# Optimization experiments

Measured on AMD Instinct MI355X. Metric: run time of the kernel, lower is better.

## Reference

```python
import jax, jax.numpy as jnp
import numpy as np
from jax import lax

RADIUS = 4
HIDDEN = 64
CORR_CH = (2 * RADIUS + 1) ** 2  # 81


def _conv3x3(x, w, b):
    # x: [B, Cin, H, W], w: [Cout, Cin, 3, 3], b: [Cout]
    y = lax.conv_general_dilated(
        x, w, window_strides=(1, 1), padding='SAME',
        dimension_numbers=('NCHW', 'OIHW', 'NCHW'))
    return y + b[None, :, None, None]


def setup_inputs() -> dict:
    key = jax.random.key(0)
    ks = jax.random.split(key, 8)
    B, C, H, W = 8, 256, 128, 128
    F1 = jax.random.normal(ks[0], (B, C, H, W), dtype=jnp.float32)
    F2 = jax.random.normal(ks[1], (B, C, H, W), dtype=jnp.float32)
    # refine_net params (PyTorch Conv2d default init scale ~ 1/sqrt(fan_in))
    def conv_init(k, cout, cin):
        bound = 1.0 / np.sqrt(cin * 9)
        kw, kb = jax.random.split(k)
        w = jax.random.uniform(kw, (cout, cin, 3, 3), jnp.float32, -bound, bound)
        b = jax.random.uniform(kb, (cout,), jnp.float32, -bound, bound)
        return w, b
    w1, b1 = conv_init(ks[2], HIDDEN, CORR_CH)
    w2, b2 = conv_init(ks[3], HIDDEN, HIDDEN)
    w3, b3 = conv_init(ks[4], 2, HIDDEN)
    return {'F1': F1, 'F2': F2, 'w1': w1, 'b1': b1, 'w2': w2, 'b2': b2,
            'w3': w3, 'b3': b3}


def local_correlation(F1, F2, radius=RADIUS):
    # Correlation volume: for each (dy, dx) in the (2r+1)^2 window,
    # corr[:, k] = sum_c F1 * roll(F2, (dy, dx)) / sqrt(C).
    C = F1.shape[1]
    scale = 1.0 / np.sqrt(C).astype(np.float32)
    corr_planes = []
    for dy in range(-radius, radius + 1):
        for dx in range(-radius, radius + 1):
            shifted = jnp.roll(F2, shift=(dy, dx), axis=(2, 3))
            corr_planes.append(jnp.sum(F1 * shifted, axis=1) * scale)
    return jnp.stack(corr_planes, axis=1)  # [B, 81, H, W]


def reference(F1, F2, w1, b1, w2, b2, w3, b3):
    corr = local_correlation(F1, F2)
    h = jax.nn.relu(_conv3x3(corr, w1, b1))
    h = jax.nn.relu(_conv3x3(h, w2, b2))
    flow = _conv3x3(h, w3, b3)  # [B, 2, H, W]
    return flow
```

## Files before the change

### kernel.cpp

```cpp
#include <hip/hip_runtime.h>

typedef _Float16 half_t;
typedef _Float16 half8 __attribute__((ext_vector_type(8)));
typedef float float4v __attribute__((ext_vector_type(4)));

constexpr int NB = 8, NC = 256, NH = 128, NW = 128;
constexpr int XPAD = 130;
constexpr int C1 = 96;

__global__ void prep_weights_kernel(const float* __restrict__ w1,
                                    const float* __restrict__ w2,
                                    const float* __restrict__ w3,
                                    half_t* __restrict__ WtX1,
                                    half_t* __restrict__ WtX2,
                                    half_t* __restrict__ WtX3) {
  int stride = gridDim.x * blockDim.x;
  int i0 = blockIdx.x * blockDim.x + threadIdx.x;
  for (int i = i0; i < 27 * 64 * 32; i += stride) {
    int s = i >> 11, r = i & 2047, co = r >> 5, cq = r & 31;
    int kykx = s / 3, ci = (s % 3) * 32 + cq;
    int ky = kykx / 3, kx = kykx % 3;
    float v = (ci < 81) ? w1[((co * 81 + ci) * 3 + ky) * 3 + kx] : 0.f;
    WtX1[i] = (half_t)v;
  }
  for (int i = i0; i < 18 * 64 * 32; i += stride) {
    int s = i >> 11, r = i & 2047, co = r >> 5, cq = r & 31;
    int kykx = s >> 1, ci = (s & 1) * 32 + cq;
    int ky = kykx / 3, kx = kykx % 3;
    WtX2[i] = (half_t)w2[((co * 64 + ci) * 3 + ky) * 3 + kx];
  }
  for (int i = i0; i < 18 * 16 * 32; i += stride) {
    int s = i >> 9, r = i & 511, co = r >> 5, cq = r & 31;
    int kykx = s >> 1, ci = (s & 1) * 32 + cq;
    int ky = kykx / 3, kx = kykx % 3;
    float v = (co < 2) ? w3[((co * 64 + ci) * 3 + ky) * 3 + kx] : 0.f;
    WtX3[i] = (half_t)v;
  }
}

__global__ __launch_bounds__(256) void nhwc_kernel(const float* __restrict__ F2,
                                                   half_t* __restrict__ F2n) {
  int v = blockIdx.x * 256 + threadIdx.x;
  int x = v & 127, y = (v >> 7) & 127, cg = (v >> 14) & 31, b = v >> 19;
  const float* sp = F2 + (((size_t)(b * NC + cg * 8) * NH + y) * NW + x);
  half8 h;
#pragma unroll
  for (int j = 0; j < 8; ++j) h[j] = (half_t)sp[(size_t)j * NH * NW];
  *(half8*)(F2n + (((size_t)(b * NH + y) * NW + x) * NC + cg * 8)) = h;
}

__global__ __launch_bounds__(512) void corr_kernel(const float* __restrict__ F1,
                                                   const half_t* __restrict__ F2n,
                                                   half_t* __restrict__ corr) {
  int bid = blockIdx.x;
  int b = bid & 7, y = bid >> 3;
  int tid = threadIdx.x, wave = tid >> 6, lane = tid & 63;
  int q = lane >> 4, l15 = lane & 15;
  int x0w = wave * 16, xB = x0w + l15;

  float4v acc[9][2];
#pragma unroll
  for (int i = 0; i < 9; ++i)
#pragma unroll
    for (int j = 0; j < 2; ++j)
#pragma unroll
      for (int e = 0; e < 4; ++e) acc[i][j][e] = 0.f;

  const float* F1b = F1 + (size_t)b * NC * NH * NW + (size_t)y * NW + xB;
  const half_t* F2b = F2n + (size_t)b * NH * NW * NC;

  int x1 = (x0w - 4 + l15) & 127;
  int x2 = (x0w + 12 + l15) & 127;

  int rowoff[9];
#pragma unroll
  for (int r = 0; r < 9; ++r) rowoff[r] = ((y - 4 + r) & 127) * NW * NC;

  for (int c0 = 0; c0 < NC; c0 += 32) {
    half8 bf;
#pragma unroll
    for (int j = 0; j < 8; ++j) bf[j] = (half_t)F1b[(size_t)(c0 + q * 8 + j) * (NH * NW)];
#pragma unroll
    for (int dyi = 0; dyi < 9; ++dyi) {
      const half_t* rp = F2b + rowoff[8 - dyi] + c0 + q * 8;
      half8 a1 = *(const half8*)(rp + x1 * NC);
      half8 a2 = *(const half8*)(rp + x2 * NC);
      acc[dyi][0] = __builtin_amdgcn_mfma_f32_16x16x32_f16(a1, bf, acc[dyi][0], 0, 0, 0);
      acc[dyi][1] = __builtin_amdgcn_mfma_f32_16x16x32_f16(a2, bf, acc[dyi][1], 0, 0, 0);
    }
  }

  half_t* pbase = corr + ((size_t)(b * NH + y) * XPAD + xB + 1) * C1;
  int top1 = l15 + 8 - 4 * q;
  int top2 = l15 - 8 - 4 * q;
#pragma unroll
  for (int dyi = 0; dyi < 9; ++dyi) {
#pragma unroll
    for (int e = 0; e < 4; ++e) {
      int d1 = top1 - e;
      if (d1 >= 0 && d1 <= 8) pbase[dyi * 9 + d1] = (half_t)(acc[dyi][0][e] * 0.0625f);
      int d2 = top2 - e;
      if (d2 >= 0 && d2 <= 8) pbase[dyi * 9 + d2] = (half_t)(acc[dyi][1][e] * 0.0625f);
    }
  }
  if (q == 0) {
    pbase[81] = (half_t)0.f;
#pragma unroll
    for (int k = 0; k < 7; ++k) *(unsigned int*)((char*)pbase + 164 + 4 * k) = 0u;
  }
  if (tid < 48) {
    int slot = (tid < 24) ? 0 : 129;
    int o = tid % 24;
    half_t* pp = corr + ((size_t)(b * NH + y) * XPAD + slot) * C1;
    *(unsigned long long*)((char*)pp + o * 8) = 0ull;
  }
}

template <int CIN, int KSPL, bool RELU>
__global__ __launch_bounds__(256) void conv_kernel(const half_t* __restrict__ src,
                                                   const half_t* __restrict__ WtX,
                                                   const float* __restrict__ bias,
                                                   half_t* __restrict__ dst) {
  int bid = blockIdx.x;
  int b = bid & 7, y = bid >> 3;
  int tid = threadIdx.x, w = tid >> 6, lane = tid & 63;
  int q = lane >> 4, l15 = lane & 15;
  int xh = (w & 1) * 64, coh = (w >> 1) * 32;

  float4v acc[2][4];
#pragma unroll
  for (int i = 0; i < 2; ++i)
#pragma unroll
    for (int j = 0; j < 4; ++j)
#pragma unroll
      for (int e = 0; e < 4; ++e) acc[i][j][e] = 0.f;

  const half_t* srcb = src + (size_t)(b * NH) * XPAD * CIN;
  const half_t* wp = WtX + (coh + l15) * 32 + q * 8;
  int xb = xh + l15 + 1;

#pragma unroll
  for (int s = 0; s < 9 * KSPL; ++s) {
    int kykx = s / KSPL, ci0 = (s % KSPL) * 32;
    int dy = kykx / 3 - 1, dx = kykx % 3 - 1;
    int ty = y + dy;
    if ((unsigned)ty < (unsigned)NH) {
      half8 a0 = *(const half8*)(wp + s * 2048);
      half8 a1 = *(const half8*)(wp + s * 2048 + 512);
      const half_t* rp = srcb + (size_t)ty * XPAD * CIN + ci0 + q * 8;
#pragma unroll
      for (int nf = 0; nf < 4; ++nf) {
        half8 bf = *(const half8*)(rp + (size_t)(xb + nf * 16 + dx) * CIN);
        acc[0][nf] = __builtin_amdgcn_mfma_f32_16x16x32_f16(a0, bf, acc[0][nf], 0, 0, 0);
        acc[1][nf] = __builtin_amdgcn_mfma_f32_16x16x32_f16(a1, bf, acc[1][nf], 0, 0, 0);
      }
    }
  }

  half_t* drow = dst + (size_t)(b * NH + y) * XPAD * 64;
#pragma unroll
  for (int mf = 0; mf < 2; ++mf) {
    int co = coh + mf * 16 + q * 4;
    float4v bv = *(const float4v*)(bias + co);
#pragma unroll
    for (int nf = 0; nf < 4; ++nf) {
      int x = xh + nf * 16 + l15;
      union { half_t h[4]; unsigned long long u; } pk;
#pragma unroll
      for (int e = 0; e < 4; ++e) {
        float v = acc[mf][nf][e] + bv[e];
        if (RELU) v = v > 0.f ? v : 0.f;
        pk.h[e] = (half_t)v;
      }
      *(unsigned long long*)(drow + (size_t)(x + 1) * 64 + co) = pk.u;
    }
  }
  if (tid < 32) {
    int slot = (tid < 16) ? 0 : 129;
    int o = tid & 15;
    *(unsigned long long*)((char*)(drow + (size_t)slot * 64) + o * 8) = 0ull;
  }
}

__global__ __launch_bounds__(256) void conv3_kernel(const half_t* __restrict__ h2,
                                                    const half_t* __restrict__ WtX3,
                                                    const float* __restrict__ b3,
                                                    float* __restrict__ out) {
  int bid = blockIdx.x;
  int b = bid & 7, y0 = (bid >> 3) * 2;
  int tid = threadIdx.x, w = tid >> 6, lane = tid & 63;
  int q = lane >> 4, l15 = lane & 15;
  int y = y0 + (w >> 1), xh = (w & 1) * 64;

  half8 a[18];
#pragma unroll
  for (int s = 0; s < 18; ++s) a[s] = *(const half8*)(WtX3 + (s * 16 + l15) * 32 + q * 8);

  float4v acc[4];
#pragma unroll
  for (int j = 0; j < 4; ++j)
#pragma unroll
    for (int e = 0; e < 4; ++e) acc[j][e] = 0.f;

  const half_t* hb = h2 + (size_t)(b * NH) * XPAD * 64;
#pragma unroll
  for (int s = 0; s < 18; ++s) {
    int kykx = s >> 1, ci0 = (s & 1) * 32;
    int dy = kykx / 3 - 1, dx = kykx % 3 - 1;
    int ty = y + dy;
    if ((unsigned)ty < (unsigned)NH) {
      const half_t* rp = hb + (size_t)ty * XPAD * 64 + ci0 + q * 8;
#pragma unroll
      for (int nf = 0; nf < 4; ++nf) {
        half8 bf = *(const half8*)(rp + (size_t)(xh + nf * 16 + l15 + 1 + dx) * 64);
        acc[nf] = __builtin_amdgcn_mfma_f32_16x16x32_f16(a[s], bf, acc[nf], 0, 0, 0);
      }
    }
  }

  if (q == 0) {
    float c0v = b3[0], c1v = b3[1];
#pragma unroll
    for (int nf = 0; nf < 4; ++nf) {
      int x = xh + nf * 16 + l15;
      out[((size_t)(b * 2 + 0) * NH + y) * NW + x] = acc[nf][0] + c0v;
      out[((size_t)(b * 2 + 1) * NH + y) * NW + x] = acc[nf][1] + c1v;
    }
  }
}

extern "C" void kernel_launch(void* const* d_in, const int* in_sizes, int n_in,
                              void* d_out, int out_size, void* d_ws, size_t ws_size,
                              hipStream_t stream) {
  const float* F1 = (const float*)d_in[0];
  const float* F2 = (const float*)d_in[1];
  const float* w1 = (const float*)d_in[2];
  const float* b1 = (const float*)d_in[3];
  const float* w2 = (const float*)d_in[4];
  const float* b2 = (const float*)d_in[5];
  const float* w3 = (const float*)d_in[6];
  const float* b3 = (const float*)d_in[7];
  float* out = (float*)d_out;

  char* ws = (char*)d_ws;
  const size_t f2n_bytes = (size_t)NB * NH * NW * NC * 2;
  const size_t corr_bytes = (size_t)NB * NH * XPAD * C1 * 2;
  const size_t h_bytes = (size_t)NB * NH * XPAD * 64 * 2;

  half_t* F2n = (half_t*)ws;
  half_t* corr = (half_t*)(ws + f2n_bytes);
  half_t* h1 = (half_t*)ws;
  half_t* h2 = (half_t*)(ws + h_bytes);
  char* wbase = ws + f2n_bytes + corr_bytes;
  half_t* WtX1 = (half_t*)wbase;
  half_t* WtX2 = (half_t*)(wbase + 110592);
  half_t* WtX3 = (half_t*)(wbase + 110592 + 73728);

  prep_weights_kernel<<<64, 256, 0, stream>>>(w1, w2, w3, WtX1, WtX2, WtX3);
  nhwc_kernel<<<16384, 256, 0, stream>>>(F2, F2n);
  corr_kernel<<<1024, 512, 0, stream>>>(F1, F2n, corr);
  conv_kernel<96, 3, true><<<1024, 256, 0, stream>>>(corr, WtX1, b1, h1);
  conv_kernel<64, 2, true><<<1024, 256, 0, stream>>>(h1, WtX2, b2, h2);
  conv3_kernel<<<512, 256, 0, stream>>>(h2, WtX3, b3, out);
}
```

Before: 600.1 us.

## Restructure correlation loop and stage F2 NHWC transpose through swizzled LDS

The NHWC transpose kernel now loads a 128-pixel by 64-channel tile per block, stages it in XOR-swizzled shared memory, and writes contiguous 16-byte channel vectors. This replaces per-thread strided scattered stores. The correlation kernel preloads all F1 fragments for 256 channels into registers once, then loops over rows with only two accumulators, storing each row right away instead of holding 18 accumulators. The second x window now overlaps the first (offset 4 instead of 12), with masking to avoid duplicate writes. This trades accumulator pressure for more held B fragments and adds a 4-blocks occupancy hint.

```diff
diff --git a/kernel.cpp b/kernel.cpp
--- a/kernel.cpp
+++ b/kernel.cpp
@@ -40,73 +40,88 @@
 
 __global__ __launch_bounds__(256) void nhwc_kernel(const float* __restrict__ F2,
                                                    half_t* __restrict__ F2n) {
-  int v = blockIdx.x * 256 + threadIdx.x;
-  int x = v & 127, y = (v >> 7) & 127, cg = (v >> 14) & 31, b = v >> 19;
-  const float* sp = F2 + (((size_t)(b * NC + cg * 8) * NH + y) * NW + x);
-  half8 h;
-#pragma unroll
-  for (int j = 0; j < 8; ++j) h[j] = (half_t)sp[(size_t)j * NH * NW];
-  *(half8*)(F2n + (((size_t)(b * NH + y) * NW + x) * NC + cg * 8)) = h;
-}
-
-__global__ __launch_bounds__(512) void corr_kernel(const float* __restrict__ F1,
-                                                   const half_t* __restrict__ F2n,
-                                                   half_t* __restrict__ corr) {
+  __shared__ __align__(16) half_t T[128 * 64];
+  int bid = blockIdx.x;
+  int y = bid & 127, cq = (bid >> 7) & 3, b = bid >> 9;
+  int tid = threadIdx.x;
+
+  const float* src = F2 + ((size_t)(b * NC + cq * 64) * NH + y) * NW;
+#pragma unroll
+  for (int k = 0; k < 4; ++k) {
+    int u = tid + k * 256;
+    int px = u & 127, c8 = u >> 7;
+    half8 h;
+#pragma unroll
+    for (int j = 0; j < 8; ++j) h[j] = (half_t)src[(size_t)(c8 * 8 + j) * (NH * NW) + px];
+    int byt = (px * 128 + c8 * 16) ^ ((px & 7) << 4);
+    *(half8*)((char*)T + byt) = h;
+  }
+  __syncthreads();
+  half_t* dst = F2n + ((size_t)(b * NH + y) * NW) * NC + cq * 64;
+#pragma unroll
+  for (int k = 0; k < 4; ++k) {
+    int u = tid + k * 256;
+    int c8 = u & 7, px = u >> 3;
+    int byt = (px * 128 + c8 * 16) ^ ((px & 7) << 4);
+    *(half8*)(dst + (size_t)px * NC + c8 * 8) = *(const half8*)((const char*)T + byt);
+  }
+}
+
+__global__ __launch_bounds__(512, 4) void corr_kernel(const float* __restrict__ F1,
+                                                      const half_t* __restrict__ F2n,
+                                                      half_t* __restrict__ corr) {
   int bid = blockIdx.x;
   int b = bid & 7, y = bid >> 3;
   int tid = threadIdx.x, wave = tid >> 6, lane = tid & 63;
   int q = lane >> 4, l15 = lane & 15;
   int x0w = wave * 16, xB = x0w + l15;
 
-  float4v acc[9][2];
-#pragma unroll
-  for (int i = 0; i < 9; ++i)
-#pragma unroll
-    for (int j = 0; j < 2; ++j)
-#pragma unroll
-      for (int e = 0; e < 4; ++e) acc[i][j][e] = 0.f;
-
-  const float* F1b = F1 + (size_t)b * NC * NH * NW + (size_t)y * NW + xB;
-  const half_t* F2b = F2n + (size_t)b * NH * NW * NC;
-
+  const float* F1p = F1 + (size_t)b * NC * NH * NW + (size_t)y * NW + xB;
+  half8 bfr[8];
+#pragma unroll
+  for (int c = 0; c < 8; ++c) {
+    half8 t;
+#pragma unroll
+    for (int j = 0; j < 8; ++j) t[j] = (half_t)F1p[(size_t)(c * 32 + q * 8 + j) * (NH * NW)];
+    bfr[c] = t;
+  }
+
+  const half_t* F2b = F2n + (size_t)b * NH * NW * NC + q * 8;
   int x1 = (x0w - 4 + l15) & 127;
-  int x2 = (x0w + 12 + l15) & 127;
-
-  int rowoff[9];
-#pragma unroll
-  for (int r = 0; r < 9; ++r) rowoff[r] = ((y - 4 + r) & 127) * NW * NC;
-
-  for (int c0 = 0; c0 < NC; c0 += 32) {
-    half8 bf;
-#pragma unroll
-    for (int j = 0; j < 8; ++j) bf[j] = (half_t)F1b[(size_t)(c0 + q * 8 + j) * (NH * NW)];
-#pragma unroll
-    for (int dyi = 0; dyi < 9; ++dyi) {
-      const half_t* rp = F2b + rowoff[8 - dyi] + c0 + q * 8;
-      half8 a1 = *(const half8*)(rp + x1 * NC);
-      half8 a2 = *(const half8*)(rp + x2 * NC);
-      acc[dyi][0] = __builtin_amdgcn_mfma_f32_16x16x32_f16(a1, bf, acc[dyi][0], 0, 0, 0);
-      acc[dyi][1] = __builtin_amdgcn_mfma_f32_16x16x32_f16(a2, bf, acc[dyi][1], 0, 0, 0);
-    }
-  }
-
-  half_t* pbase = corr + ((size_t)(b * NH + y) * XPAD + xB + 1) * C1;
-  int top1 = l15 + 8 - 4 * q;
-  int top2 = l15 - 8 - 4 * q;
-#pragma unroll
-  for (int dyi = 0; dyi < 9; ++dyi) {
+  int x2 = (x0w + 4 + l15) & 127;
+  const half_t* p1 = F2b + (size_t)x1 * NC;
+  const half_t* p2 = F2b + (size_t)x2 * NC;
+
+  half_t* pb0 = corr + ((size_t)(b * NH + y) * XPAD + xB + 1) * C1;
+  int dbase = l15 - 4 * q;
+
+#pragma unroll
+  for (int r = 0; r < 9; ++r) {
+    size_t ro = (size_t)((y - 4 + r) & 127) * (NW * NC);
+    float4v a0, a1;
+#pragma unroll
+    for (int e = 0; e < 4; ++e) { a0[e] = 0.f; a1[e] = 0.f; }
+#pragma unroll
+    for (int c = 0; c < 8; ++c) {
+      half8 f1 = *(const half8*)(p1 + ro + c * 32);
+      half8 f2 = *(const half8*)(p2 + ro + c * 32);
+      a0 = __builtin_amdgcn_mfma_f32_16x16x32_f16(f1, bfr[c], a0, 0, 0, 0);
+      a1 = __builtin_amdgcn_mfma_f32_16x16x32_f16(f2, bfr[c], a1, 0, 0, 0);
+    }
+    half_t* pb = pb0 + (8 - r) * 9;
 #pragma unroll
     for (int e = 0; e < 4; ++e) {
-      int d1 = top1 - e;
-      if (d1 >= 0 && d1 <= 8) pbase[dyi * 9 + d1] = (half_t)(acc[dyi][0][e] * 0.0625f);
-      int d2 = top2 - e;
-      if (d2 >= 0 && d2 <= 8) pbase[dyi * 9 + d2] = (half_t)(acc[dyi][1][e] * 0.0625f);
-    }
-  }
+      int d1 = dbase - e + 8;
+      if (q < 2 && (unsigned)d1 <= 8u) pb[d1] = (half_t)(a0[e] * 0.0625f);
+      int d2 = dbase - e;
+      if ((unsigned)d2 <= 8u) pb[d2] = (half_t)(a1[e] * 0.0625f);
+    }
+  }
+
   if (q == 0) {
-    pbase[81] = (half_t)0.f;
-#pragma unroll
-    for (int k = 0; k < 7; ++k) *(unsigned int*)((char*)pbase + 164 + 4 * k) = 0u;
+    pb0[81] = (half_t)0.f;
+#pragma unroll
+    for (int k = 0; k < 7; ++k) *(unsigned int*)((char*)pb0 + 164 + 4 * k) = 0u;
   }
   if (tid < 48) {
     int slot = (tid < 24) ? 0 : 129;
@@ -257,7 +272,7 @@
   half_t* WtX3 = (half_t*)(wbase + 110592 + 73728);
 
   prep_weights_kernel<<<64, 256, 0, stream>>>(w1, w2, w3, WtX1, WtX2, WtX3);
-  nhwc_kernel<<<16384, 256, 0, stream>>>(F2, F2n);
+  nhwc_kernel<<<4096, 256, 0, stream>>>(F2, F2n);
   corr_kernel<<<1024, 512, 0, stream>>>(F1, F2n, corr);
   conv_kernel<96, 3, true><<<1024, 256, 0, stream>>>(corr, WtX1, b1, h1);
   conv_kernel<64, 2, true><<<1024, 256, 0, stream>>>(h1, WtX2, b2, h2);
```

After: 587.3 us. -2.1%, faster.
